# Performance work log

Hardware: AMD Instinct MI355X
Metric: run time of the kernel (lower is better)

The kernel has to match this reference:

```python
import jax, jax.numpy as jnp
import numpy as np

B, N, IN_DIM, HID = 16, 2048, 128, 128
EPS = 1e-5


def _layer(x, W, b, g, beta):
    # x: (B, N, d_in) -> (B, N, HID)
    h = jnp.einsum('bnd,dh->bnh', x, W) + b
    mu = jnp.mean(h, axis=-1, keepdims=True)
    var = jnp.mean((h - mu) ** 2, axis=-1, keepdims=True)
    h = (h - mu) * jax.lax.rsqrt(var + EPS) * g + beta
    return jax.nn.relu(h)


def setup_inputs() -> dict:
    key = jax.random.key(0)
    ks = jax.random.split(key, 8)
    x = jax.random.normal(ks[0], (B, N, IN_DIM), dtype=jnp.float32)
    adj = jax.random.uniform(ks[1], (B, N, N), dtype=jnp.float32)
    inp = {'x': x, 'adj': adj}
    dims = [IN_DIM, HID, HID]
    for i in range(3):
        d_in = dims[i]
        scale = 1.0 / np.sqrt(d_in)
        inp[f'W{i}'] = jax.random.uniform(ks[2 + i], (d_in, HID), dtype=jnp.float32, minval=-scale, maxval=scale)
        inp[f'b{i}'] = jax.random.uniform(ks[5 + i], (HID,), dtype=jnp.float32, minval=-scale, maxval=scale)
        inp[f'g{i}'] = jnp.ones((HID,), dtype=jnp.float32)
        inp[f'be{i}'] = jnp.zeros((HID,), dtype=jnp.float32)
    return inp


def reference(x, adj, W0, b0, g0, be0, W1, b1, g1, be1, W2, b2, g2, be2):
    params = [(W0, b0, g0, be0), (W1, b1, g1, be1), (W2, b2, g2, be2)]
    h = x
    for (W, b, g, beta) in params:
        h_agg = jnp.einsum('bnm,bmd->bnd', adj, h)  # dense adjacency aggregation
        h = _layer(h_agg, W, b, g, beta)
    return h
```

## Files before the change

### kernel.cpp

```cpp
#include <hip/hip_runtime.h>
#include <hip/hip_bf16.h>

typedef __bf16 bf16;
typedef __bf16 bf16x8 __attribute__((ext_vector_type(8)));
typedef float  f32x4  __attribute__((ext_vector_type(4)));

static constexpr int NB  = 16;
static constexpr int NN  = 2048;
static constexpr int HID = 128;

__device__ __forceinline__ void gload_lds16(const bf16* g, bf16* l) {
    __builtin_amdgcn_global_load_lds(
        (const __attribute__((address_space(1))) unsigned int*)g,
        (__attribute__((address_space(3))) unsigned int*)l, 16, 0, 0);
}

#define WAITV(n) asm volatile("s_waitcnt vmcnt(" #n ")" ::: "memory")


__global__ __launch_bounds__(256) void prep_wt(const float* __restrict__ W0,
                                               const float* __restrict__ W1,
                                               const float* __restrict__ W2,
                                               bf16* __restrict__ WTg) {
    int l = blockIdx.x;
    const float* W = (l == 0) ? W0 : (l == 1) ? W1 : W2;
    bf16* out = WTg + l * 16384;
    int tid = threadIdx.x;
#pragma unroll
    for (int i = 0; i < 8; ++i) {
        int p = i * 256 + tid;
        int n = p >> 4, half = (p >> 3) & 1, cs = p & 7;
        int kc = cs ^ (n & 7);
        int kbase = half * 64 + kc * 8;
        bf16x8 o;
#pragma unroll
        for (int r = 0; r < 8; ++r) o[r] = (bf16)W[(kbase + r) * 128 + n];
        *(bf16x8*)(out + p * 8) = o;
    }
}

__global__ __launch_bounds__(256) void prep_xt(const float* __restrict__ x,
                                               bf16* __restrict__ xTt) {
    __shared__ bf16 T[128 * 136];
    const int blk = blockIdx.x;
    const int b = blk >> 4, node0 = (blk & 15) * 128;
    const int tid = threadIdx.x;
    const float* xb = x + ((size_t)b * NN + node0) * HID;
#pragma unroll
    for (int i = 0; i < 64; ++i) {
        int idx = i * 256 + tid;
        int node = idx >> 7, hid = idx & 127;
        T[hid * 136 + node] = (bf16)xb[(size_t)node * HID + hid];
    }
    __syncthreads();
#pragma unroll
    for (int i = 0; i < 8; ++i) {
        int p = i * 256 + tid;
        int half = p >> 10, p1 = p & 1023;
        int n = p1 >> 3, cs = p1 & 7, c = cs ^ (n & 7), m = half * 64 + c * 8;
        *(bf16x8*)(xTt + ((size_t)b * 32 + (node0 >> 6) + half) * 8192 + p1 * 8)
            = *(const bf16x8*)(T + n * 136 + m);
    }
}

template<int AMODE, bool FINAL>
__global__ __launch_bounds__(256, 2) void layer64(
        const float* __restrict__ Af, bf16* __restrict__ adjT,
        const bf16* __restrict__ Bt, const bf16* __restrict__ WTg,
        const float* __restrict__ bias, const float* __restrict__ gam,
        const float* __restrict__ bet, bf16* __restrict__ hOut,
        float* __restrict__ outF) {
    __shared__ __align__(16) bf16 lds[36864];

    const int tid = threadIdx.x, wave = tid >> 6, lane = tid & 63;
    const int c0 = lane & 15, q = lane >> 4;
    const int blk = blockIdx.x, xcd = blk & 7, jj = blk >> 3;
    const int b = xcd * 2 + (jj & 1);
    const int mt = jj >> 1, m0 = mt * 64;

    const bf16* Btb = Bt + (size_t)b * 32 * 8192;
    bf16* Atl = adjT + ((size_t)b * 32 + mt) * (size_t)(32 * 4096);
    const float* Afb = Af + (size_t)b * NN * NN + (size_t)m0 * NN;

    f32x4 acc[8] = {};

    auto stageA = [&](int buf, int kk) {
#pragma unroll
        for (int j = 0; j < 2; ++j) {
            int cb = j * 256 + wave * 64;
            gload_lds16(Atl + (size_t)kk * 4096 + (size_t)(cb + lane) * 8,
                        lds + buf * 12288 + cb * 8);
        }
    };
    auto stageB = [&](int buf, int kk) {
#pragma unroll
        for (int j = 0; j < 4; ++j) {
            int cb = j * 256 + wave * 64;
            gload_lds16(Btb + (size_t)kk * 8192 + (size_t)(cb + lane) * 8,
                        lds + buf * 12288 + 4096 + cb * 8);
        }
    };

    int g_row[2], g_cb[2];
#pragma unroll
    for (int j = 0; j < 2; ++j) {
        int gi = j * 256 + tid;
        g_row[j] = gi >> 3; g_cb[j] = gi & 7;
    }
    f32x4 va[2], vb[2];
    auto loadA = [&](int kk) {
#pragma unroll
        for (int j = 0; j < 2; ++j) {
            const float* s = Afb + (size_t)g_row[j] * NN + kk * 64 + g_cb[j] * 8;
            va[j] = *(const f32x4*)s;
            vb[j] = *(const f32x4*)(s + 4);
        }
    };
    auto writeA = [&](int buf, int kk) {
#pragma unroll
        for (int j = 0; j < 2; ++j) {
            bf16x8 o = {(bf16)va[j].x, (bf16)va[j].y, (bf16)va[j].z, (bf16)va[j].w,
                        (bf16)vb[j].x, (bf16)vb[j].y, (bf16)vb[j].z, (bf16)vb[j].w};
            int ch = g_row[j] * 8 + (g_cb[j] ^ (g_row[j] & 7));
            *(bf16x8*)(lds + buf * 12288 + ch * 8) = o;
            *(bf16x8*)(Atl + (size_t)kk * 4096 + ch * 8) = o;
        }
    };
    auto compute = [&](int buf) {
        const bf16* As = lds + buf * 12288;
        const bf16* Bs = As + 4096;
#pragma unroll
        for (int ks = 0; ks < 2; ++ks) {
            int kb = ks * 4 + q;
            int ar = wave * 16 + c0;
            bf16x8 af = *(const bf16x8*)(As + ar * 64 + (kb ^ (ar & 7)) * 8);
#pragma unroll
            for (int nt = 0; nt < 8; ++nt) {
                int br = nt * 16 + c0;
                bf16x8 bw = *(const bf16x8*)(Bs + br * 64 + (kb ^ (br & 7)) * 8);
                acc[nt] = __builtin_amdgcn_mfma_f32_16x16x32_bf16(af, bw, acc[nt], 0, 0, 0);
            }
        }
    };

    if constexpr (AMODE == 1) {
        loadA(0); writeA(0, 0); stageB(0, 0);
        loadA(1); writeA(1, 1); stageB(1, 1);
    } else {
        stageA(0, 0); stageB(0, 0);
        stageA(1, 1); stageB(1, 1);
    }

    int bufk = 0;
#pragma unroll 1
    for (int kk = 0; kk < 32; ++kk) {
        if (kk < 31) WAITV(6);
        else         WAITV(0);
        __builtin_amdgcn_s_barrier();
        const int b2 = bufk ? bufk - 1 : 2;
        if constexpr (AMODE == 1) {
            if (kk < 30) loadA(kk + 2);
            compute(bufk);
            if (kk < 30) { writeA(b2, kk + 2); stageB(b2, kk + 2); }
        } else {
            compute(bufk);
            if (kk < 30) { stageA(b2, kk + 2); stageB(b2, kk + 2); }
        }
        bufk = (bufk == 2) ? 0 : bufk + 1;
    }
    __syncthreads();

    bf16* G = lds;
#pragma unroll
    for (int nt = 0; nt < 8; ++nt)
#pragma unroll
        for (int r = 0; r < 4; ++r) {
            int row = wave * 16 + q * 4 + r;
            G[row * 136 + nt * 16 + c0] = (bf16)acc[nt][r];
        }
    __syncthreads();

    f32x4 a2[8] = {};
    {
        const int gr = wave * 16 + c0;
#pragma unroll
        for (int ks = 0; ks < 4; ++ks) {
            bf16x8 af = *(const bf16x8*)(G + gr * 136 + ks * 32 + q * 8);
#pragma unroll
            for (int nt = 0; nt < 8; ++nt) {
                int n = nt * 16 + c0;
                int ch = n * 16 + (ks >> 1) * 8 + ((((ks & 1) << 2) | q) ^ (n & 7));
                bf16x8 bw = *(const bf16x8*)(WTg + (size_t)ch * 8);
                a2[nt] = __builtin_amdgcn_mfma_f32_16x16x32_bf16(af, bw, a2[nt], 0, 0, 0);
            }
        }
    }

    float bv[8], gv[8], ev[8];
#pragma unroll
    for (int nt = 0; nt < 8; ++nt) {
        int n = nt * 16 + c0;
        bv[nt] = bias[n]; gv[nt] = gam[n]; ev[nt] = bet[n];
    }
    bf16* Cs = lds;
    if constexpr (!FINAL) __syncthreads();
#pragma unroll
    for (int r = 0; r < 4; ++r) {
        float v[8], s1 = 0.f, s2 = 0.f;
#pragma unroll
        for (int nt = 0; nt < 8; ++nt) {
            float xv = a2[nt][r] + bv[nt];
            v[nt] = xv; s1 += xv; s2 += xv * xv;
        }
#pragma unroll
        for (int off = 1; off < 16; off <<= 1) {
            s1 += __shfl_xor(s1, off);
            s2 += __shfl_xor(s2, off);
        }
        float mu = s1 * (1.f / 128.f);
        float var = s2 * (1.f / 128.f) - mu * mu;
        float rs = rsqrtf(var + 1e-5f);
        int row = wave * 16 + q * 4 + r;
        if constexpr (FINAL) {
            size_t ro = ((size_t)b * NN + m0 + row) * HID;
#pragma unroll
            for (int nt = 0; nt < 8; ++nt) {
                float o = fmaxf((v[nt] - mu) * rs * gv[nt] + ev[nt], 0.f);
                outF[ro + nt * 16 + c0] = o;
            }
        } else {
#pragma unroll
            for (int nt = 0; nt < 8; ++nt) {
                float o = fmaxf((v[nt] - mu) * rs * gv[nt] + ev[nt], 0.f);
                Cs[(nt * 16 + c0) * 72 + row] = (bf16)o;
            }
        }
    }
    if constexpr (!FINAL) {
        __syncthreads();
#pragma unroll
        for (int i = 0; i < 4; ++i) {
            int p1 = i * 256 + tid;
            int n = p1 >> 3, cs = p1 & 7, c = cs ^ (n & 7), m = c * 8;
            *(bf16x8*)(hOut + ((size_t)b * 32 + mt) * 8192 + p1 * 8)
                = *(const bf16x8*)(Cs + n * 72 + m);
        }
    }
}

extern "C" void kernel_launch(void* const* d_in, const int* in_sizes, int n_in,
                              void* d_out, int out_size, void* d_ws, size_t ws_size,
                              hipStream_t stream) {
    const float* x   = (const float*)d_in[0];
    const float* adj = (const float*)d_in[1];
    const float* W[3]  = {(const float*)d_in[2],  (const float*)d_in[6],  (const float*)d_in[10]};
    const float* bb[3] = {(const float*)d_in[3],  (const float*)d_in[7],  (const float*)d_in[11]};
    const float* gg[3] = {(const float*)d_in[4],  (const float*)d_in[8],  (const float*)d_in[12]};
    const float* be[3] = {(const float*)d_in[5],  (const float*)d_in[9],  (const float*)d_in[13]};

    char* ws = (char*)d_ws;
    size_t off = 0;
    auto alloc = [&](size_t bytes) {
        char* p = ws + off; off = (off + bytes + 255) & ~(size_t)255; return p;
    };
    bf16* WTg  = (bf16*)alloc((size_t)3 * 16384 * 2);
    bf16* xTt  = (bf16*)alloc((size_t)NB * 32 * 8192 * 2);
    bf16* hT0  = (bf16*)alloc((size_t)NB * 32 * 8192 * 2);
    bf16* hT1  = (bf16*)alloc((size_t)NB * 32 * 8192 * 2);
    bf16* adjT = (bf16*)alloc((size_t)NB * 32 * 32 * 4096 * 2);

    float* outF = (float*)d_out;

    prep_wt<<<3, 256, 0, stream>>>(W[0], W[1], W[2], WTg);
    prep_xt<<<256, 256, 0, stream>>>(x, xTt);

    layer64<1, false><<<512, 256, 0, stream>>>(adj, adjT, xTt, WTg,
                                               bb[0], gg[0], be[0], hT0, nullptr);
    layer64<2, false><<<512, 256, 0, stream>>>(adj, adjT, hT0, WTg + 16384,
                                               bb[1], gg[1], be[1], hT1, nullptr);
    layer64<2, true ><<<512, 256, 0, stream>>>(adj, adjT, hT1, WTg + 2 * 16384,
                                               bb[2], gg[2], be[2], nullptr, outF);
}
```

Baseline: 513.9 us.

## Shrink layer tiles to 32 rows with 2-wave blocks and double buffering

Each layer block now covers 32 adjacency rows with 128 threads instead of 64 rows with 256, so the grid doubles to 1024 blocks and more blocks can be resident per CU. The triple-buffered LDS pipeline becomes double-buffered with extra barriers, and the layer-0 path changes to a simpler prefetch-then-sync loop. The aim is better occupancy and load balance on the memory-bound fp32 adjacency read and conversion. The cost is that B-operand (h) tiles are re-read from L2 twice as often, each wave must issue more B staging loads, and the shallower pipeline hides less latency.

After: 550.2 us. +7.1%, slower.

```diff
diff --git a/kernel.cpp b/kernel.cpp
--- a/kernel.cpp
+++ b/kernel.cpp
@@ -64,22 +64,22 @@
 }
 
 template<int AMODE, bool FINAL>
-__global__ __launch_bounds__(256, 2) void layer64(
+__global__ __launch_bounds__(128, 2) void layer32(
         const float* __restrict__ Af, bf16* __restrict__ adjT,
         const bf16* __restrict__ Bt, const bf16* __restrict__ WTg,
         const float* __restrict__ bias, const float* __restrict__ gam,
         const float* __restrict__ bet, bf16* __restrict__ hOut,
         float* __restrict__ outF) {
-    __shared__ __align__(16) bf16 lds[36864];
+    __shared__ __align__(16) bf16 lds[20480];
 
     const int tid = threadIdx.x, wave = tid >> 6, lane = tid & 63;
     const int c0 = lane & 15, q = lane >> 4;
     const int blk = blockIdx.x, xcd = blk & 7, jj = blk >> 3;
     const int b = xcd * 2 + (jj & 1);
-    const int mt = jj >> 1, m0 = mt * 64;
+    const int mt = jj >> 1, m0 = mt * 32;
 
     const bf16* Btb = Bt + (size_t)b * 32 * 8192;
-    bf16* Atl = adjT + ((size_t)b * 32 + mt) * (size_t)(32 * 4096);
+    bf16* Atl = adjT + ((size_t)b * 64 + mt) * (size_t)(32 * 2048);
     const float* Afb = Af + (size_t)b * NN * NN + (size_t)m0 * NN;
 
     f32x4 acc[8] = {};
@@ -87,48 +87,22 @@
     auto stageA = [&](int buf, int kk) {
 #pragma unroll
         for (int j = 0; j < 2; ++j) {
-            int cb = j * 256 + wave * 64;
-            gload_lds16(Atl + (size_t)kk * 4096 + (size_t)(cb + lane) * 8,
-                        lds + buf * 12288 + cb * 8);
+            int cb = j * 128 + wave * 64;
+            gload_lds16(Atl + (size_t)kk * 2048 + (size_t)(cb + lane) * 8,
+                        lds + buf * 10240 + cb * 8);
         }
     };
     auto stageB = [&](int buf, int kk) {
 #pragma unroll
-        for (int j = 0; j < 4; ++j) {
-            int cb = j * 256 + wave * 64;
+        for (int j = 0; j < 8; ++j) {
+            int cb = j * 128 + wave * 64;
             gload_lds16(Btb + (size_t)kk * 8192 + (size_t)(cb + lane) * 8,
-                        lds + buf * 12288 + 4096 + cb * 8);
-        }
-    };
-
-    int g_row[2], g_cb[2];
-#pragma unroll
-    for (int j = 0; j < 2; ++j) {
-        int gi = j * 256 + tid;
-        g_row[j] = gi >> 3; g_cb[j] = gi & 7;
-    }
-    f32x4 va[2], vb[2];
-    auto loadA = [&](int kk) {
-#pragma unroll
-        for (int j = 0; j < 2; ++j) {
-            const float* s = Afb + (size_t)g_row[j] * NN + kk * 64 + g_cb[j] * 8;
-            va[j] = *(const f32x4*)s;
-            vb[j] = *(const f32x4*)(s + 4);
-        }
-    };
-    auto writeA = [&](int buf, int kk) {
-#pragma unroll
-        for (int j = 0; j < 2; ++j) {
-            bf16x8 o = {(bf16)va[j].x, (bf16)va[j].y, (bf16)va[j].z, (bf16)va[j].w,
-                        (bf16)vb[j].x, (bf16)vb[j].y, (bf16)vb[j].z, (bf16)vb[j].w};
-            int ch = g_row[j] * 8 + (g_cb[j] ^ (g_row[j] & 7));
-            *(bf16x8*)(lds + buf * 12288 + ch * 8) = o;
-            *(bf16x8*)(Atl + (size_t)kk * 4096 + ch * 8) = o;
+                        lds + buf * 10240 + 2048 + cb * 8);
         }
     };
     auto compute = [&](int buf) {
-        const bf16* As = lds + buf * 12288;
-        const bf16* Bs = As + 4096;
+        const bf16* As = lds + buf * 10240;
+        const bf16* Bs = As + 2048;
 #pragma unroll
         for (int ks = 0; ks < 2; ++ks) {
             int kb = ks * 4 + q;
@@ -144,31 +118,57 @@
     };
 
     if constexpr (AMODE == 1) {
-        loadA(0); writeA(0, 0); stageB(0, 0);
-        loadA(1); writeA(1, 1); stageB(1, 1);
+        int grow[2], gcb[2];
+#pragma unroll
+        for (int j = 0; j < 2; ++j) {
+            int gi = j * 128 + tid;
+            grow[j] = gi >> 3; gcb[j] = gi & 7;
+        }
+        f32x4 va[2], vb[2];
+        auto loadA = [&](int kk) {
+#pragma unroll
+            for (int j = 0; j < 2; ++j) {
+                const float* s = Afb + (size_t)grow[j] * NN + kk * 64 + gcb[j] * 8;
+                va[j] = *(const f32x4*)s;
+                vb[j] = *(const f32x4*)(s + 4);
+            }
+        };
+        auto writeA = [&](int buf, int kk) {
+#pragma unroll
+            for (int j = 0; j < 2; ++j) {
+                bf16x8 o = {(bf16)va[j].x, (bf16)va[j].y, (bf16)va[j].z, (bf16)va[j].w,
+                            (bf16)vb[j].x, (bf16)vb[j].y, (bf16)vb[j].z, (bf16)vb[j].w};
+                int ch = grow[j] * 8 + (gcb[j] ^ (grow[j] & 7));
+                *(bf16x8*)(lds + buf * 10240 + ch * 8) = o;
+                *(bf16x8*)(Atl + (size_t)kk * 2048 + ch * 8) = o;
+            }
+        };
+        loadA(0); stageB(0, 0); writeA(0, 0);
+        __syncthreads();
+        int cur = 0;
+        for (int kk = 0; kk < 32; ++kk) {
+            if (kk < 31) { loadA(kk + 1); stageB(cur ^ 1, kk + 1); }
+            compute(cur);
+            if (kk < 31) writeA(cur ^ 1, kk + 1);
+            __syncthreads();
+            cur ^= 1;
+        }
     } else {
         stageA(0, 0); stageB(0, 0);
         stageA(1, 1); stageB(1, 1);
-    }
-
-    int bufk = 0;
 #pragma unroll 1
-    for (int kk = 0; kk < 32; ++kk) {
-        if (kk < 31) WAITV(6);
-        else         WAITV(0);
-        __builtin_amdgcn_s_barrier();
-        const int b2 = bufk ? bufk - 1 : 2;
-        if constexpr (AMODE == 1) {
-            if (kk < 30) loadA(kk + 2);
-            compute(bufk);
-            if (kk < 30) { writeA(b2, kk + 2); stageB(b2, kk + 2); }
-        } else {
-            compute(bufk);
-            if (kk < 30) { stageA(b2, kk + 2); stageB(b2, kk + 2); }
-        }
-        bufk = (bufk == 2) ? 0 : bufk + 1;
-    }
-    __syncthreads();
+        for (int kk = 0; kk < 32; ++kk) {
+            if (kk < 31) WAITV(10);
+            else         WAITV(0);
+            __builtin_amdgcn_s_barrier();
+            asm volatile("" ::: "memory");
+            compute(kk & 1);
+            asm volatile("" ::: "memory");
+            __builtin_amdgcn_s_barrier();
+            if (kk < 30) { stageA(kk & 1, kk + 2); stageB(kk & 1, kk + 2); }
+        }
+        __syncthreads();
+    }
 
     bf16* G = lds;
 #pragma unroll
@@ -232,18 +232,21 @@
 #pragma unroll
             for (int nt = 0; nt < 8; ++nt) {
                 float o = fmaxf((v[nt] - mu) * rs * gv[nt] + ev[nt], 0.f);
-                Cs[(nt * 16 + c0) * 72 + row] = (bf16)o;
+                Cs[(nt * 16 + c0) * 40 + row] = (bf16)o;
             }
         }
     }
     if constexpr (!FINAL) {
         __syncthreads();
+        const int kkb = mt >> 1, kc0 = (mt & 1) * 4;
+        bf16* outp = hOut + ((size_t)b * 32 + kkb) * 8192;
 #pragma unroll
         for (int i = 0; i < 4; ++i) {
-            int p1 = i * 256 + tid;
-            int n = p1 >> 3, cs = p1 & 7, c = cs ^ (n & 7), m = c * 8;
-            *(bf16x8*)(hOut + ((size_t)b * 32 + mt) * 8192 + p1 * 8)
-                = *(const bf16x8*)(Cs + n * 72 + m);
+            int idx = i * 128 + tid;
+            int n = idx >> 2, kco = idx & 3;
+            int kc = kc0 + kco;
+            int chunk = n * 8 + (kc ^ (n & 7));
+            *(bf16x8*)(outp + chunk * 8) = *(const bf16x8*)(Cs + n * 40 + kco * 8);
         }
     }
 }
@@ -267,17 +270,17 @@
     bf16* xTt  = (bf16*)alloc((size_t)NB * 32 * 8192 * 2);
     bf16* hT0  = (bf16*)alloc((size_t)NB * 32 * 8192 * 2);
     bf16* hT1  = (bf16*)alloc((size_t)NB * 32 * 8192 * 2);
-    bf16* adjT = (bf16*)alloc((size_t)NB * 32 * 32 * 4096 * 2);
+    bf16* adjT = (bf16*)alloc((size_t)NB * 64 * 32 * 2048 * 2);
 
     float* outF = (float*)d_out;
 
     prep_wt<<<3, 256, 0, stream>>>(W[0], W[1], W[2], WTg);
     prep_xt<<<256, 256, 0, stream>>>(x, xTt);
 
-    layer64<1, false><<<512, 256, 0, stream>>>(adj, adjT, xTt, WTg,
-                                               bb[0], gg[0], be[0], hT0, nullptr);
-    layer64<2, false><<<512, 256, 0, stream>>>(adj, adjT, hT0, WTg + 16384,
-                                               bb[1], gg[1], be[1], hT1, nullptr);
-    layer64<2, true ><<<512, 256, 0, stream>>>(adj, adjT, hT1, WTg + 2 * 16384,
-                                               bb[2], gg[2], be[2], nullptr, outF);
-}
+    layer32<1, false><<<1024, 128, 0, stream>>>(adj, adjT, xTt, WTg,
+                                                bb[0], gg[0], be[0], hT0, nullptr);
+    layer32<2, false><<<1024, 128, 0, stream>>>(adj, adjT, hT0, WTg + 16384,
+                                                bb[1], gg[1], be[1], hT1, nullptr);
+    layer32<2, true ><<<1024, 128, 0, stream>>>(adj, adjT, hT1, WTg + 2 * 16384,
+                                                bb[2], gg[2], be[2], nullptr, outF);
+}
```
